# Kernel optimization log

Hardware: AMD Instinct MI355X
Metric: run time of the kernel (lower is better)

## Reference

```python
import jax, jax.numpy as jnp
import numpy as np

N_NODES = 50000
N_EDGES = 800000
IN_DIM, FEAT_DIM, HID_DIM, OUT_DIM = 512, 256, 256, 128


def _glorot(key, shape):
    fan_in = shape[-1]
    bound = 1.0 / np.sqrt(fan_in)
    return jax.random.uniform(key, shape, jnp.float32, -bound, bound)


def setup_inputs() -> dict:
    key = jax.random.key(0)
    ks = jax.random.split(key, 12)
    x = jax.random.normal(ks[0], (N_NODES, IN_DIM), jnp.float32)
    edge_index = jax.random.randint(ks[1], (2, N_EDGES), 0, N_NODES, jnp.int64)
    return {
        "x": x,
        "edge_index": edge_index,
        # feature_pre MLP
        "W_pre": _glorot(ks[2], (FEAT_DIM, IN_DIM)),
        "b_pre": jnp.zeros((FEAT_DIM,), jnp.float32),
        "W_pre2": _glorot(ks[3], (HID_DIM, FEAT_DIM)),
        "b_pre2": jnp.zeros((HID_DIM,), jnp.float32),
        # conv_first: SAGEConv(hidden, hidden); lin_l (neighbors, with bias), lin_r (root, no bias)
        "Wl1": _glorot(ks[4], (HID_DIM, HID_DIM)),
        "bl1": jnp.zeros((HID_DIM,), jnp.float32),
        "Wr1": _glorot(ks[5], (HID_DIM, HID_DIM)),
        # conv_out: SAGEConv(hidden, output)
        "Wl2": _glorot(ks[6], (OUT_DIM, HID_DIM)),
        "bl2": jnp.zeros((OUT_DIM,), jnp.float32),
        "Wr2": _glorot(ks[7], (OUT_DIM, HID_DIM)),
    }


def sage_conv(x, src, dst, Wl, bl, Wr):
    # mean-aggregate source features at destination nodes, then linear + root linear
    n = x.shape[0]
    msg = x[src]                                               # [E, D]
    agg = jax.ops.segment_sum(msg, dst, num_segments=n)        # [N, D]
    cnt = jax.ops.segment_sum(jnp.ones((src.shape[0],), x.dtype), dst, num_segments=n)
    mean = agg / jnp.maximum(cnt, 1.0)[:, None]
    return mean @ Wl.T + bl + x @ Wr.T


def reference(x, edge_index, W_pre, b_pre, W_pre2, b_pre2, Wl1, bl1, Wr1, Wl2, bl2, Wr2):
    src, dst = edge_index[0], edge_index[1]
    h = x @ W_pre.T + b_pre
    h = h @ W_pre2.T + b_pre2
    h = jax.nn.relu(sage_conv(h, src, dst, Wl1, bl1, Wr1))
    # dropout is identity in eval mode; layer_num=2 -> no hidden convs
    h = sage_conv(h, src, dst, Wl2, bl2, Wr2)
    # F.normalize(p=2, dim=-1), eps=1e-12
    norm = jnp.maximum(jnp.linalg.norm(h, axis=-1, keepdims=True), 1e-12)
    return h / norm
```

## Files before the change

kernel.cpp:

```cpp
#include <hip/hip_runtime.h>
#include <hip/hip_bf16.h>


typedef __attribute__((ext_vector_type(4))) float f32x4;
typedef __attribute__((ext_vector_type(8))) short s8v;

#define A_BUF_SZ 8192
#define B_BUF_SZ 32768
#define B_BASE   (2 * A_BUF_SZ)

__device__ __forceinline__ float bf2f(unsigned short u) {
  union { unsigned int i; float f; } v; v.i = ((unsigned int)u) << 16; return v.f;
}
__device__ __forceinline__ unsigned short f2bf(float f) {
  unsigned int u = __builtin_bit_cast(unsigned int, f);
  u += 0x7fffu + ((u >> 16) & 1u);
  return (unsigned short)(u >> 16);
}

__global__ __launch_bounds__(256) void zero_int_kernel(int* __restrict__ p, int n) {
  int i = blockIdx.x * blockDim.x + threadIdx.x;
  const int stride = gridDim.x * blockDim.x;
  for (; i < n; i += stride) p[i] = 0;
}

__global__ __launch_bounds__(256) void count_kernel(const int* __restrict__ dst,
                                                    int* __restrict__ cnt, int E) {
  const int e = blockIdx.x * blockDim.x + threadIdx.x;
  if (e < E) atomicAdd(&cnt[dst[e]], 1);
}

__global__ __launch_bounds__(256) void scan_pass1(const int* __restrict__ cnt,
                                                  int* __restrict__ bsum, int M) {
  __shared__ int red[256];
  const int t = threadIdx.x;
  const int i = blockIdx.x * 256 + t;
  red[t] = (i < M) ? cnt[i] : 0;
  __syncthreads();
  for (int off = 128; off > 0; off >>= 1) {
    if (t < off) red[t] += red[t + off];
    __syncthreads();
  }
  if (t == 0) bsum[blockIdx.x] = red[0];
}

__global__ __launch_bounds__(256) void scan_pass2(const int* __restrict__ bsum,
    int* __restrict__ boff, int* __restrict__ rowptr, int nb, int M, int E) {
  __shared__ int buf[256];
  const int t = threadIdx.x;
  const int v = (t < nb) ? bsum[t] : 0;
  buf[t] = v;
  __syncthreads();
  for (int off = 1; off < 256; off <<= 1) {
    const int add = (t >= off) ? buf[t - off] : 0;
    __syncthreads();
    buf[t] += add;
    __syncthreads();
  }
  if (t < nb) boff[t] = buf[t] - v;
  if (t == 0) rowptr[M] = E;
}

__global__ __launch_bounds__(256) void scan_pass3(int* __restrict__ cnt,
    const int* __restrict__ boff, int* __restrict__ rowptr, int M) {
  __shared__ int buf[256];
  const int t = threadIdx.x;
  const int i = blockIdx.x * 256 + t;
  const int v = (i < M) ? cnt[i] : 0;
  buf[t] = v;
  __syncthreads();
  for (int off = 1; off < 256; off <<= 1) {
    const int add = (t >= off) ? buf[t - off] : 0;
    __syncthreads();
    buf[t] += add;
    __syncthreads();
  }
  if (i < M) {
    rowptr[i] = buf[t] - v + boff[blockIdx.x];
    cnt[i] = 0;
  }
}

__global__ __launch_bounds__(256) void fill_kernel(const int* __restrict__ src,
    const int* __restrict__ dst, const int* __restrict__ rowptr,
    int* __restrict__ cursor, unsigned short* __restrict__ eidx, int E) {
  const int e = blockIdx.x * blockDim.x + threadIdx.x;
  if (e >= E) return;
  const int d = dst[e];
  const int pos = rowptr[d] + atomicAdd(&cursor[d], 1);
  eidx[pos] = (unsigned short)src[e];
}

__global__ __launch_bounds__(256) void prep_kernel(const float* __restrict__ Wp,
    const float* __restrict__ Wp2, const float* __restrict__ bp,
    const float* __restrict__ bp2, const float* __restrict__ Wl1,
    const float* __restrict__ Wr1, const float* __restrict__ Wl2,
    const float* __restrict__ Wr2, unsigned short* __restrict__ Wc,
    float* __restrict__ bc, unsigned short* __restrict__ Bc1,
    unsigned short* __restrict__ Bc2) {
  const int b = blockIdx.x, t = threadIdx.x;
  if (b < 256) {
    __shared__ float wrow[256];
    wrow[t] = Wp2[b * 256 + t];
    __syncthreads();
    float a0 = 0.f, a1 = 0.f;
    for (int m = 0; m < 256; ++m) {
      const float w = wrow[m];
      a0 = fmaf(w, Wp[m * 512 + t], a0);
      a1 = fmaf(w, Wp[m * 512 + 256 + t], a1);
    }
    Wc[b * 512 + t] = f2bf(a0);
    Wc[b * 512 + 256 + t] = f2bf(a1);
  } else if (b == 256) {
    float s = 0.f;
    for (int m = 0; m < 256; ++m) s = fmaf(Wp2[t * 256 + m], bp[m], s);
    bc[t] = s + bp2[t];
  } else if (b < 769) {
    const int idx = (b - 257) * 256 + t;
    const int o = idx >> 9, k = idx & 511;
    const float v = (k < 256) ? Wl1[o * 256 + k] : Wr1[o * 256 + (k - 256)];
    Bc1[idx] = f2bf(v);
  } else {
    const int idx = (b - 769) * 256 + t;
    const int r = idx >> 8, k = idx & 255;
    const float v = (r < 128) ? Wl2[r * 256 + k] : Wr2[(r - 128) * 256 + k];
    Bc2[idx] = f2bf(v);
  }
}

template <int K, int ASTRIDE, int CSTRIDE, int CBASE, bool BIAS_EN, bool RELU_EN, bool A_FP32>
__global__ __launch_bounds__(256) void mfma_gemm(const void* __restrict__ Ap,
    const unsigned short* __restrict__ Bp, const float* __restrict__ bias,
    unsigned short* __restrict__ Cp, int M) {
  constexpr int NT = K / 64;
  __shared__ __align__(16) char smem[2 * A_BUF_SZ + 2 * B_BUF_SZ];

  const int t = threadIdx.x, w = t >> 6, l = t & 63;
  const int bm = blockIdx.x * 64;
  const int lane15 = l & 15, half = (l >> 4) & 3;

  float bias_l[4];
  if (BIAS_EN) {
#pragma unroll
    for (int ns = 0; ns < 4; ++ns) bias_l[ns] = bias[w * 64 + ns * 16 + lane15];
  }

  f32x4 acc[4][4];
#pragma unroll
  for (int i = 0; i < 4; ++i)
#pragma unroll
    for (int j = 0; j < 4; ++j) acc[i][j] = f32x4{0.f, 0.f, 0.f, 0.f};

  auto stageB = [&](char* dstB, int k0) {
#pragma unroll
    for (int i = 0; i < 8; ++i) {
      const int c = i * 256 + t;
      const int rB = c >> 3;
      const int sl = (c & 7) ^ (rB & 7);
      __builtin_amdgcn_global_load_lds(
          (const unsigned int*)(Bp + (size_t)rB * K + k0 + sl * 8),
          (unsigned int*)(dstB + i * 4096 + w * 1024), 16, 0, 0);
    }
  };
  auto stageA_bf16 = [&](char* dstA, int k0) {
#pragma unroll
    for (int i = 0; i < 2; ++i) {
      const int c = w * 128 + i * 64 + l;
      const int rA = c >> 3;
      const int sl = (c & 7) ^ (rA & 7);
      const unsigned short* ap = (const unsigned short*)Ap +
          (size_t)min(bm + rA, M - 1) * ASTRIDE + k0 + sl * 8;
      __builtin_amdgcn_global_load_lds((const unsigned int*)ap,
          (unsigned int*)(dstA + w * 2048 + i * 1024), 16, 0, 0);
    }
  };
  const int rAf = t >> 2;
  const int arowf = min(bm + rAf, M - 1);
  const int phys0 = ((t & 3) * 2) ^ (rAf & 7);
  auto loadA_f32 = [&](int k0, float4* ar) {
    const float* ap = (const float*)Ap + (size_t)arowf * ASTRIDE + k0 + (t & 3) * 16;
    ar[0] = *(const float4*)(ap + 0);
    ar[1] = *(const float4*)(ap + 4);
    ar[2] = *(const float4*)(ap + 8);
    ar[3] = *(const float4*)(ap + 12);
  };
  auto writeA_f32 = [&](char* dstA, const float4* ar) {
    s8v p0, p1;
    p0[0] = (short)f2bf(ar[0].x); p0[1] = (short)f2bf(ar[0].y);
    p0[2] = (short)f2bf(ar[0].z); p0[3] = (short)f2bf(ar[0].w);
    p0[4] = (short)f2bf(ar[1].x); p0[5] = (short)f2bf(ar[1].y);
    p0[6] = (short)f2bf(ar[1].z); p0[7] = (short)f2bf(ar[1].w);
    p1[0] = (short)f2bf(ar[2].x); p1[1] = (short)f2bf(ar[2].y);
    p1[2] = (short)f2bf(ar[2].z); p1[3] = (short)f2bf(ar[2].w);
    p1[4] = (short)f2bf(ar[3].x); p1[5] = (short)f2bf(ar[3].y);
    p1[6] = (short)f2bf(ar[3].z); p1[7] = (short)f2bf(ar[3].w);
    *(s8v*)(dstA + (rAf * 8 + phys0) * 16) = p0;
    *(s8v*)(dstA + (rAf * 8 + (phys0 ^ 1)) * 16) = p1;
  };

  stageB(smem + B_BASE, 0);
  if (A_FP32) {
    float4 ar[4];
    loadA_f32(0, ar);
    writeA_f32(smem, ar);
  } else {
    stageA_bf16(smem, 0);
  }
  __syncthreads();

  int cur = 0;
#pragma unroll 1
  for (int tt = 0; tt < NT; ++tt) {
    char* const Ac = smem + cur * A_BUF_SZ;
    char* const Bc = smem + B_BASE + cur * B_BUF_SZ;
    char* const An = smem + (cur ^ 1) * A_BUF_SZ;
    char* const Bn = smem + B_BASE + (cur ^ 1) * B_BUF_SZ;
    const bool more = (tt + 1 < NT);

    float4 ar[4];
    if (more) {
      stageB(Bn, (tt + 1) * 64);
      if (A_FP32) loadA_f32((tt + 1) * 64, ar);
      else stageA_bf16(An, (tt + 1) * 64);
    }

#pragma unroll
    for (int ksub = 0; ksub < 2; ++ksub) {
      const int spx = (ksub * 4 + half) ^ (lane15 & 7);
      s8v af[4], bv[4];
#pragma unroll
      for (int ms = 0; ms < 4; ++ms)
        af[ms] = *(const s8v*)(Ac + (ms * 16 + lane15) * 128 + spx * 16);
#pragma unroll
      for (int ns = 0; ns < 4; ++ns)
        bv[ns] = *(const s8v*)(Bc + (w * 64 + ns * 16 + lane15) * 128 + spx * 16);
#pragma unroll
      for (int ms = 0; ms < 4; ++ms)
#pragma unroll
        for (int ns = 0; ns < 4; ++ns)
          acc[ms][ns] =
              __builtin_amdgcn_mfma_f32_16x16x32_bf16(af[ms], bv[ns], acc[ms][ns], 0, 0, 0);
    }

    if (more) {
      if (A_FP32) writeA_f32(An, ar);
      __syncthreads();
    }
    cur ^= 1;
  }

#pragma unroll
  for (int ms = 0; ms < 4; ++ms)
#pragma unroll
    for (int ns = 0; ns < 4; ++ns) {
      const int col = w * 64 + ns * 16 + lane15;
      f32x4 v = acc[ms][ns];
      if (BIAS_EN) {
#pragma unroll
        for (int r = 0; r < 4; ++r) v[r] += bias_l[ns];
      }
      if (RELU_EN) {
#pragma unroll
        for (int r = 0; r < 4; ++r) v[r] = fmaxf(v[r], 0.f);
      }
#pragma unroll
      for (int r = 0; r < 4; ++r) {
        const int row = bm + ms * 16 + half * 4 + r;
        if (row < M) Cp[(size_t)row * CSTRIDE + CBASE + col] = f2bf(v[r]);
      }
    }
}

__global__ __launch_bounds__(256) void gather_mean256_kernel(
    unsigned short* __restrict__ Acat, const int* __restrict__ rowptr,
    const unsigned short* __restrict__ eidx, int M) {
  const int node = blockIdx.x * 4 + (threadIdx.x >> 6);
  if (node >= M) return;
  const int lane = threadIdx.x & 63;
  const int c4 = lane * 4;
  const int beg = rowptr[node], end = rowptr[node + 1];
  float a0 = 0.f, a1 = 0.f, a2 = 0.f, a3 = 0.f;
  int j = beg;
  for (; j + 3 < end; j += 4) {
    const size_t s0 = eidx[j], s1 = eidx[j + 1], s2 = eidx[j + 2], s3 = eidx[j + 3];
    const ushort4 v0 = *(const ushort4*)(Acat + s0 * 512 + 256 + c4);
    const ushort4 v1 = *(const ushort4*)(Acat + s1 * 512 + 256 + c4);
    const ushort4 v2 = *(const ushort4*)(Acat + s2 * 512 + 256 + c4);
    const ushort4 v3 = *(const ushort4*)(Acat + s3 * 512 + 256 + c4);
    a0 += (bf2f(v0.x) + bf2f(v1.x)) + (bf2f(v2.x) + bf2f(v3.x));
    a1 += (bf2f(v0.y) + bf2f(v1.y)) + (bf2f(v2.y) + bf2f(v3.y));
    a2 += (bf2f(v0.z) + bf2f(v1.z)) + (bf2f(v2.z) + bf2f(v3.z));
    a3 += (bf2f(v0.w) + bf2f(v1.w)) + (bf2f(v2.w) + bf2f(v3.w));
  }
  for (; j < end; ++j) {
    const size_t s0 = eidx[j];
    const ushort4 v0 = *(const ushort4*)(Acat + s0 * 512 + 256 + c4);
    a0 += bf2f(v0.x); a1 += bf2f(v0.y); a2 += bf2f(v0.z); a3 += bf2f(v0.w);
  }
  const float inv = 1.0f / fmaxf((float)(end - beg), 1.0f);
  ushort4 o;
  o.x = f2bf(a0 * inv); o.y = f2bf(a1 * inv);
  o.z = f2bf(a2 * inv); o.w = f2bf(a3 * inv);
  *(ushort4*)(Acat + (size_t)node * 512 + c4) = o;
}

__global__ __launch_bounds__(256) void gather_finalize_kernel(
    const unsigned short* __restrict__ Acat, const int* __restrict__ rowptr,
    const unsigned short* __restrict__ eidx, const float* __restrict__ bl2,
    float* __restrict__ out, int M) {
  const int node = blockIdx.x * 4 + (threadIdx.x >> 6);
  if (node >= M) return;
  const int lane = threadIdx.x & 63;
  const int c2 = lane * 2;
  const int beg = rowptr[node], end = rowptr[node + 1];
  float ax = 0.f, ay = 0.f;
  int j = beg;
  for (; j + 3 < end; j += 4) {
    const size_t s0 = eidx[j], s1 = eidx[j + 1], s2 = eidx[j + 2], s3 = eidx[j + 3];
    const ushort2 v0 = *(const ushort2*)(Acat + s0 * 512 + 256 + c2);
    const ushort2 v1 = *(const ushort2*)(Acat + s1 * 512 + 256 + c2);
    const ushort2 v2 = *(const ushort2*)(Acat + s2 * 512 + 256 + c2);
    const ushort2 v3 = *(const ushort2*)(Acat + s3 * 512 + 256 + c2);
    ax += (bf2f(v0.x) + bf2f(v1.x)) + (bf2f(v2.x) + bf2f(v3.x));
    ay += (bf2f(v0.y) + bf2f(v1.y)) + (bf2f(v2.y) + bf2f(v3.y));
  }
  for (; j < end; ++j) {
    const size_t s0 = eidx[j];
    const ushort2 v0 = *(const ushort2*)(Acat + s0 * 512 + 256 + c2);
    ax += bf2f(v0.x); ay += bf2f(v0.y);
  }
  const float inv = 1.0f / fmaxf((float)(end - beg), 1.0f);
  const ushort2 rr = *(const ushort2*)(Acat + (size_t)node * 512 + 384 + c2);
  const float2 b = *(const float2*)&bl2[c2];
  const float vx = fmaf(ax, inv, b.x) + bf2f(rr.x);
  const float vy = fmaf(ay, inv, b.y) + bf2f(rr.y);
  float ss = vx * vx + vy * vy;
#pragma unroll
  for (int off = 32; off > 0; off >>= 1) ss += __shfl_xor(ss, off);
  const float rn = 1.0f / fmaxf(sqrtf(ss), 1e-12f);
  *(float2*)&out[(size_t)node * 128 + c2] = make_float2(vx * rn, vy * rn);
}

extern "C" void kernel_launch(void* const* d_in, const int* in_sizes, int n_in,
                              void* d_out, int out_size, void* d_ws, size_t ws_size,
                              hipStream_t stream) {
  const float* x      = (const float*)d_in[0];
  const int*   ei     = (const int*)d_in[1];
  const float* W_pre  = (const float*)d_in[2];
  const float* b_pre  = (const float*)d_in[3];
  const float* W_pre2 = (const float*)d_in[4];
  const float* b_pre2 = (const float*)d_in[5];
  const float* Wl1    = (const float*)d_in[6];
  const float* bl1    = (const float*)d_in[7];
  const float* Wr1    = (const float*)d_in[8];
  const float* Wl2    = (const float*)d_in[9];
  const float* bl2    = (const float*)d_in[10];
  const float* Wr2    = (const float*)d_in[11];
  float* out = (float*)d_out;

  const int M = in_sizes[0] / 512;
  const int E = in_sizes[1] / 2;
  const int* src = ei;
  const int* dst = ei + E;

  char* p = (char*)d_ws;
  unsigned short* Acat = (unsigned short*)p; p += (size_t)M * 512 * 2;
  unsigned short* H3   = (unsigned short*)p; p += (size_t)M * 256 * 2;
  unsigned short* Wc   = (unsigned short*)p; p += 256 * 512 * 2;
  unsigned short* Bc1  = (unsigned short*)p; p += 256 * 512 * 2;
  unsigned short* Bc2  = (unsigned short*)p; p += 256 * 256 * 2;
  float* bc   = (float*)p; p += 256 * 4;
  int* rowptr = (int*)p;   p += (size_t)(M + 1) * 4;
  int* cnt    = (int*)p;   p += (size_t)M * 4;
  int* bsum   = (int*)p;   p += 256 * 4;
  int* boff   = (int*)p;   p += 256 * 4;
  unsigned short* eidx = (unsigned short*)p;

  const int eblk = (E + 255) / 256;
  const int nb   = (M + 255) / 256;
  const int gx   = (M + 63) / 64;
  const int nblk = (M + 3) / 4;

  zero_int_kernel<<<256, 256, 0, stream>>>(cnt, M);
  count_kernel<<<eblk, 256, 0, stream>>>(dst, cnt, E);
  scan_pass1<<<nb, 256, 0, stream>>>(cnt, bsum, M);
  scan_pass2<<<1, 256, 0, stream>>>(bsum, boff, rowptr, nb, M, E);
  scan_pass3<<<nb, 256, 0, stream>>>(cnt, boff, rowptr, M);
  fill_kernel<<<eblk, 256, 0, stream>>>(src, dst, rowptr, cnt, eidx, E);

  prep_kernel<<<1025, 256, 0, stream>>>(W_pre, W_pre2, b_pre, b_pre2,
                                        Wl1, Wr1, Wl2, Wr2, Wc, bc, Bc1, Bc2);

  mfma_gemm<512, 512, 512, 256, true, false, true>
      <<<gx, 256, 0, stream>>>(x, Wc, bc, Acat, M);
  gather_mean256_kernel<<<nblk, 256, 0, stream>>>(Acat, rowptr, eidx, M);
  mfma_gemm<512, 512, 256, 0, true, true, false>
      <<<gx, 256, 0, stream>>>(Acat, Bc1, bl1, H3, M);
  mfma_gemm<256, 256, 512, 256, false, false, false>
      <<<gx, 256, 0, stream>>>(H3, Bc2, nullptr, Acat, M);
  gather_finalize_kernel<<<nblk, 256, 0, stream>>>(Acat, rowptr, eidx, bl2, out, M);
}
```

Before: 275.5 us.

## Retile GEMMs to 128x128 blocks with 2D grid and single-buffered K=32 steps

Replaces the 64-row by full-256-column GEMM tile (double-buffered, 80KB LDS, K-step 64) with a 128x128 tile over a 2D grid, a 2x2 wave layout and a single 16KB LDS buffer stepped 32 at a time along K. The smaller LDS footprint is meant to allow more resident blocks per CU and to balance A/B reuse. In exchange it drops the double-buffered prefetch, adds two barriers per K step, and reads the A rows twice across the two column blocks.

```diff
diff --git a/kernel.cpp b/kernel.cpp
--- a/kernel.cpp
+++ b/kernel.cpp
@@ -4,10 +4,6 @@
 
 typedef __attribute__((ext_vector_type(4))) float f32x4;
 typedef __attribute__((ext_vector_type(8))) short s8v;
-
-#define A_BUF_SZ 8192
-#define B_BUF_SZ 32768
-#define B_BASE   (2 * A_BUF_SZ)
 
 __device__ __forceinline__ float bf2f(unsigned short u) {
   union { unsigned int i; float f; } v; v.i = ((unsigned int)u) << 16; return v.f;
@@ -132,17 +128,23 @@
 __global__ __launch_bounds__(256) void mfma_gemm(const void* __restrict__ Ap,
     const unsigned short* __restrict__ Bp, const float* __restrict__ bias,
     unsigned short* __restrict__ Cp, int M) {
-  constexpr int NT = K / 64;
-  __shared__ __align__(16) char smem[2 * A_BUF_SZ + 2 * B_BUF_SZ];
+  __shared__ __align__(16) char smem[16384];
 
   const int t = threadIdx.x, w = t >> 6, l = t & 63;
-  const int bm = blockIdx.x * 64;
-  const int lane15 = l & 15, half = (l >> 4) & 3;
+  const int bm = blockIdx.x * 128, bn = blockIdx.y * 128;
+  const int wr = (w >> 1) * 64, wc = (w & 1) * 64;
+  const int lane15 = l & 15, half = l >> 4;
+
+  const int sr = t >> 2;
+  const int sp = t & 3;
+  const int fr = t >> 1;
+  const int fh = t & 1;
+  const int frow = min(bm + fr, M - 1);
 
   float bias_l[4];
   if (BIAS_EN) {
 #pragma unroll
-    for (int ns = 0; ns < 4; ++ns) bias_l[ns] = bias[w * 64 + ns * 16 + lane15];
+    for (int ns = 0; ns < 4; ++ns) bias_l[ns] = bias[bn + wc + ns * 16 + lane15];
   }
 
   f32x4 acc[4][4];
@@ -151,109 +153,73 @@
 #pragma unroll
     for (int j = 0; j < 4; ++j) acc[i][j] = f32x4{0.f, 0.f, 0.f, 0.f};
 
-  auto stageB = [&](char* dstB, int k0) {
-#pragma unroll
-    for (int i = 0; i < 8; ++i) {
-      const int c = i * 256 + t;
-      const int rB = c >> 3;
-      const int sl = (c & 7) ^ (rB & 7);
-      __builtin_amdgcn_global_load_lds(
-          (const unsigned int*)(Bp + (size_t)rB * K + k0 + sl * 8),
-          (unsigned int*)(dstB + i * 4096 + w * 1024), 16, 0, 0);
-    }
-  };
-  auto stageA_bf16 = [&](char* dstA, int k0) {
-#pragma unroll
-    for (int i = 0; i < 2; ++i) {
-      const int c = w * 128 + i * 64 + l;
-      const int rA = c >> 3;
-      const int sl = (c & 7) ^ (rA & 7);
-      const unsigned short* ap = (const unsigned short*)Ap +
-          (size_t)min(bm + rA, M - 1) * ASTRIDE + k0 + sl * 8;
-      __builtin_amdgcn_global_load_lds((const unsigned int*)ap,
-          (unsigned int*)(dstA + w * 2048 + i * 1024), 16, 0, 0);
-    }
-  };
-  const int rAf = t >> 2;
-  const int arowf = min(bm + rAf, M - 1);
-  const int phys0 = ((t & 3) * 2) ^ (rAf & 7);
-  auto loadA_f32 = [&](int k0, float4* ar) {
-    const float* ap = (const float*)Ap + (size_t)arowf * ASTRIDE + k0 + (t & 3) * 16;
-    ar[0] = *(const float4*)(ap + 0);
-    ar[1] = *(const float4*)(ap + 4);
-    ar[2] = *(const float4*)(ap + 8);
-    ar[3] = *(const float4*)(ap + 12);
-  };
-  auto writeA_f32 = [&](char* dstA, const float4* ar) {
-    s8v p0, p1;
-    p0[0] = (short)f2bf(ar[0].x); p0[1] = (short)f2bf(ar[0].y);
-    p0[2] = (short)f2bf(ar[0].z); p0[3] = (short)f2bf(ar[0].w);
-    p0[4] = (short)f2bf(ar[1].x); p0[5] = (short)f2bf(ar[1].y);
-    p0[6] = (short)f2bf(ar[1].z); p0[7] = (short)f2bf(ar[1].w);
-    p1[0] = (short)f2bf(ar[2].x); p1[1] = (short)f2bf(ar[2].y);
-    p1[2] = (short)f2bf(ar[2].z); p1[3] = (short)f2bf(ar[2].w);
-    p1[4] = (short)f2bf(ar[3].x); p1[5] = (short)f2bf(ar[3].y);
-    p1[6] = (short)f2bf(ar[3].z); p1[7] = (short)f2bf(ar[3].w);
-    *(s8v*)(dstA + (rAf * 8 + phys0) * 16) = p0;
-    *(s8v*)(dstA + (rAf * 8 + (phys0 ^ 1)) * 16) = p1;
-  };
-
-  stageB(smem + B_BASE, 0);
-  if (A_FP32) {
-    float4 ar[4];
-    loadA_f32(0, ar);
-    writeA_f32(smem, ar);
-  } else {
-    stageA_bf16(smem, 0);
-  }
-  __syncthreads();
-
-  int cur = 0;
 #pragma unroll 1
-  for (int tt = 0; tt < NT; ++tt) {
-    char* const Ac = smem + cur * A_BUF_SZ;
-    char* const Bc = smem + B_BASE + cur * B_BUF_SZ;
-    char* const An = smem + (cur ^ 1) * A_BUF_SZ;
-    char* const Bn = smem + B_BASE + (cur ^ 1) * B_BUF_SZ;
-    const bool more = (tt + 1 < NT);
-
-    float4 ar[4];
-    if (more) {
-      stageB(Bn, (tt + 1) * 64);
-      if (A_FP32) loadA_f32((tt + 1) * 64, ar);
-      else stageA_bf16(An, (tt + 1) * 64);
-    }
-
-#pragma unroll
-    for (int ksub = 0; ksub < 2; ++ksub) {
-      const int spx = (ksub * 4 + half) ^ (lane15 & 7);
-      s8v af[4], bv[4];
-#pragma unroll
-      for (int ms = 0; ms < 4; ++ms)
-        af[ms] = *(const s8v*)(Ac + (ms * 16 + lane15) * 128 + spx * 16);
+  for (int k0 = 0; k0 < K; k0 += 32) {
+    if (k0) __syncthreads();
+    if (A_FP32) {
+      const float* ap = (const float*)Ap + (size_t)frow * ASTRIDE + k0 + fh * 8;
+      const float4 f0 = *(const float4*)(ap + 0);
+      const float4 f1 = *(const float4*)(ap + 4);
+      const float4 f2 = *(const float4*)(ap + 16);
+      const float4 f3 = *(const float4*)(ap + 20);
+      s8v p0, p1;
+      p0[0] = (short)f2bf(f0.x); p0[1] = (short)f2bf(f0.y);
+      p0[2] = (short)f2bf(f0.z); p0[3] = (short)f2bf(f0.w);
+      p0[4] = (short)f2bf(f1.x); p0[5] = (short)f2bf(f1.y);
+      p0[6] = (short)f2bf(f1.z); p0[7] = (short)f2bf(f1.w);
+      p1[0] = (short)f2bf(f2.x); p1[1] = (short)f2bf(f2.y);
+      p1[2] = (short)f2bf(f2.z); p1[3] = (short)f2bf(f2.w);
+      p1[4] = (short)f2bf(f3.x); p1[5] = (short)f2bf(f3.y);
+      p1[6] = (short)f2bf(f3.z); p1[7] = (short)f2bf(f3.w);
+      const int s1 = fh ^ (fr & 3);
+      const int s2 = (fh ^ 2) ^ (fr & 3);
+      *(s8v*)(smem + fr * 64 + s1 * 16) = p0;
+      *(s8v*)(smem + fr * 64 + s2 * 16) = p1;
+    } else {
+#pragma unroll
+      for (int j = 0; j < 2; ++j) {
+        const int r = j * 64 + sr;
+        const int sl = sp ^ (r & 3);
+        const unsigned short* ap = (const unsigned short*)Ap +
+            (size_t)min(bm + r, M - 1) * ASTRIDE + k0 + sl * 8;
+        __builtin_amdgcn_global_load_lds((const unsigned int*)ap,
+            (unsigned int*)(smem + j * 4096 + w * 1024), 16, 0, 0);
+      }
+    }
+#pragma unroll
+    for (int j = 0; j < 2; ++j) {
+      const int r = j * 64 + sr;
+      const int sl = sp ^ (r & 3);
+      const unsigned short* bp = Bp + (size_t)(bn + r) * K + k0 + sl * 8;
+      __builtin_amdgcn_global_load_lds((const unsigned int*)bp,
+          (unsigned int*)(smem + 8192 + j * 4096 + w * 1024), 16, 0, 0);
+    }
+    __syncthreads();
+
+    s8v af[4], bv[4];
+#pragma unroll
+    for (int ms = 0; ms < 4; ++ms) {
+      const int r = wr + ms * 16 + lane15;
+      af[ms] = *(const s8v*)(smem + r * 64 + (half ^ (r & 3)) * 16);
+    }
+#pragma unroll
+    for (int ns = 0; ns < 4; ++ns) {
+      const int r = wc + ns * 16 + lane15;
+      bv[ns] = *(const s8v*)(smem + 8192 + r * 64 + (half ^ (r & 3)) * 16);
+    }
+#pragma unroll
+    for (int ms = 0; ms < 4; ++ms)
 #pragma unroll
       for (int ns = 0; ns < 4; ++ns)
-        bv[ns] = *(const s8v*)(Bc + (w * 64 + ns * 16 + lane15) * 128 + spx * 16);
-#pragma unroll
-      for (int ms = 0; ms < 4; ++ms)
-#pragma unroll
-        for (int ns = 0; ns < 4; ++ns)
-          acc[ms][ns] =
-              __builtin_amdgcn_mfma_f32_16x16x32_bf16(af[ms], bv[ns], acc[ms][ns], 0, 0, 0);
-    }
-
-    if (more) {
-      if (A_FP32) writeA_f32(An, ar);
-      __syncthreads();
-    }
-    cur ^= 1;
+        acc[ms][ns] =
+            __builtin_amdgcn_mfma_f32_16x16x32_bf16(af[ms], bv[ns], acc[ms][ns], 0, 0, 0);
   }
 
 #pragma unroll
   for (int ms = 0; ms < 4; ++ms)
 #pragma unroll
     for (int ns = 0; ns < 4; ++ns) {
-      const int col = w * 64 + ns * 16 + lane15;
+      const int col = bn + wc + ns * 16 + lane15;
       f32x4 v = acc[ms][ns];
       if (BIAS_EN) {
 #pragma unroll
@@ -265,7 +231,7 @@
       }
 #pragma unroll
       for (int r = 0; r < 4; ++r) {
-        const int row = bm + ms * 16 + half * 4 + r;
+        const int row = bm + wr + ms * 16 + half * 4 + r;
         if (row < M) Cp[(size_t)row * CSTRIDE + CBASE + col] = f2bf(v[r]);
       }
     }
@@ -378,7 +344,7 @@
 
   const int eblk = (E + 255) / 256;
   const int nb   = (M + 255) / 256;
-  const int gx   = (M + 63) / 64;
+  const dim3 gg((M + 127) / 128, 2);
   const int nblk = (M + 3) / 4;
 
   zero_int_kernel<<<256, 256, 0, stream>>>(cnt, M);
@@ -392,11 +358,11 @@
                                         Wl1, Wr1, Wl2, Wr2, Wc, bc, Bc1, Bc2);
 
   mfma_gemm<512, 512, 512, 256, true, false, true>
-      <<<gx, 256, 0, stream>>>(x, Wc, bc, Acat, M);
+      <<<gg, 256, 0, stream>>>(x, Wc, bc, Acat, M);
   gather_mean256_kernel<<<nblk, 256, 0, stream>>>(Acat, rowptr, eidx, M);
   mfma_gemm<512, 512, 256, 0, true, true, false>
-      <<<gx, 256, 0, stream>>>(Acat, Bc1, bl1, H3, M);
+      <<<gg, 256, 0, stream>>>(Acat, Bc1, bl1, H3, M);
   mfma_gemm<256, 256, 512, 256, false, false, false>
-      <<<gx, 256, 0, stream>>>(H3, Bc2, nullptr, Acat, M);
+      <<<gg, 256, 0, stream>>>(H3, Bc2, nullptr, Acat, M);
   gather_finalize_kernel<<<nblk, 256, 0, stream>>>(Acat, rowptr, eidx, bl2, out, M);
 }
```

Result: slower. 307.4 us (+11.6%).
